# Kernel tuning notes

Measured on AMD Instinct MI355X. Metric: run time of the kernel, lower is better.

The kernel has to match this reference:

```python
import jax, jax.numpy as jnp
from jax import lax
import numpy as np

B, T = 16, 256
E, H, V = 512, 1024, 32000

def setup_inputs() -> dict:
    key = jax.random.key(0)
    ks = jax.random.split(key, 10)
    s = lambda fan_in: 1.0 / np.sqrt(fan_in)
    return {
        "z": jax.random.normal(ks[0], (B, H), dtype=jnp.float32),
        "x": jax.random.randint(ks[1], (B, T), 0, V, dtype=jnp.int64),
        "emb_table": jax.random.normal(ks[2], (V, E), dtype=jnp.float32) * 0.02,
        "W_init": jax.random.uniform(ks[3], (H, H), jnp.float32, -s(H), s(H)),
        "b_init": jnp.zeros((H,), jnp.float32),
        "W_ih": jax.random.uniform(ks[4], (3 * H, E), jnp.float32, -s(H), s(H)),
        "W_hh": jax.random.uniform(ks[5], (3 * H, H), jnp.float32, -s(H), s(H)),
        "b_ih": jax.random.uniform(ks[6], (3 * H,), jnp.float32, -s(H), s(H)),
        "b_hh": jax.random.uniform(ks[7], (3 * H,), jnp.float32, -s(H), s(H)),
        "W_out": jax.random.uniform(ks[8], (V, H), jnp.float32, -s(H), s(H)),
        "b_out": jnp.zeros((V,), jnp.float32),
    }

def reference(z, x, emb_table, W_init, b_init, W_ih, W_hh, b_ih, b_hh, W_out, b_out):
    # h0 = tanh(aff_init_lm(z))
    h0 = jnp.tanh(z @ W_init.T + b_init)  # [B, H]
    xe = emb_table[x]                      # [B, T, E] embedding lookup
    # Precompute input-side gate projections for all timesteps (no recurrence on input side)
    gi_all = jnp.einsum('bte,ge->btg', xe, W_ih) + b_ih  # [B, T, 3H]

    def step(h, gi):
        gh = h @ W_hh.T + b_hh                 # [B, 3H]
        ir, iz, inn = jnp.split(gi, 3, axis=-1)
        hr, hz, hn = jnp.split(gh, 3, axis=-1)
        r = jax.nn.sigmoid(ir + hr)
        zg = jax.nn.sigmoid(iz + hz)
        n = jnp.tanh(inn + r * hn)
        h_new = (1.0 - zg) * n + zg * h
        # Original module emits aff_out_x(h[j]) (state BEFORE consuming token j),
        # so we output the PREVIOUS hidden state at each step.
        return h_new, h

    _, hs_prev = lax.scan(step, h0, jnp.swapaxes(gi_all, 0, 1))  # [T, B, H] = h0..h_{T-1}
    hs = jnp.swapaxes(hs_prev, 0, 1)                              # [B, T, H]
    logits = jnp.einsum('bth,vh->btv', hs, W_out) + b_out         # [B, T, V]
    return logits
```

## Files before the change

kernel.cpp:

```cpp
#include <hip/hip_runtime.h>

typedef __attribute__((ext_vector_type(8))) short bf16x8;
typedef __attribute__((ext_vector_type(8))) unsigned short ushort8;
typedef __attribute__((ext_vector_type(4))) float f32x4;
typedef __attribute__((ext_vector_type(4))) int i32x4;

__device__ __forceinline__ unsigned short f2bf(float f) {
  union { float f; unsigned u; } v; v.f = f;
  unsigned r = (v.u + 0x7FFFu + ((v.u >> 16) & 1u)) >> 16;
  return (unsigned short)r;
}
__device__ __forceinline__ float bf2f(unsigned short h) {
  union { unsigned u; float f; } v; v.u = ((unsigned)h) << 16;
  return v.f;
}
__device__ __forceinline__ float sigm(float x) { return 1.f / (1.f + __expf(-x)); }
__device__ __forceinline__ float tanh_(float x) { return 1.f - 2.f / (__expf(2.f * x) + 1.f); }

__device__ __forceinline__ i32x4 ld_coh_b128(const void* p) {
  i32x4 r;
  asm volatile("global_load_dwordx4 %0, %1, off sc0 sc1" : "=v"(r) : "v"(p) : "memory");
  return r;
}
__device__ __forceinline__ void st_coh_b128(void* p, i32x4 v) {
  asm volatile("global_store_dwordx4 %0, %1, off sc0 sc1" :: "v"(p), "v"(v) : "memory");
}
__device__ __forceinline__ void st_coh_b16(void* p, unsigned v) {
  asm volatile("global_store_short %0, %1, off sc0 sc1" :: "v"(p), "v"(v) : "memory");
}
__device__ __forceinline__ void wait_vm0_fence() {
  asm volatile("s_waitcnt vmcnt(0)" ::: "memory");
  __builtin_amdgcn_sched_barrier(0);
}

#define GLDS(g, l) __builtin_amdgcn_global_load_lds( \
    (const __attribute__((address_space(1))) unsigned int*)(g), \
    (__attribute__((address_space(3))) unsigned int*)(l), 16, 0, 0)

__global__ __launch_bounds__(256) void prep(
    const int* __restrict__ x, const float* __restrict__ emb, unsigned short* __restrict__ xe,
    const float* __restrict__ z, const float* __restrict__ Wi, const float* __restrict__ bi,
    float* __restrict__ h0f, unsigned short* __restrict__ hb16,
    const float* __restrict__ Wih, unsigned short* __restrict__ WihB,
    const float* __restrict__ Wout, unsigned short* __restrict__ WoutB) {
  const int tid = threadIdx.x;
  const unsigned bid = blockIdx.x;
  if (bid < 2048) {
    const int m = (bid << 1) + (tid >> 7);
    const int tok = x[m];
    const int c = tid & 127;
    const float4 v = ((const float4*)(emb + (size_t)tok * 512))[c];
    ushort4 o; o.x = f2bf(v.x); o.y = f2bf(v.y); o.z = f2bf(v.z); o.w = f2bf(v.w);
    ((ushort4*)(xe + (size_t)m * 512))[c] = o;
  } else if (bid < 2112) {
    const int idx = (bid - 2048) * 256 + tid;
    const int b = idx & 15, i = idx >> 4;
    const float4* wr = (const float4*)(Wi + (size_t)i * 1024);
    const float4* zr = (const float4*)(z + (size_t)b * 1024);
    float acc = bi[i];
#pragma unroll 4
    for (int k = 0; k < 256; ++k) {
      float4 w = wr[k], zv = zr[k];
      acc += w.x * zv.x + w.y * zv.y + w.z * zv.z + w.w * zv.w;
    }
    const float h = tanh_(acc);
    h0f[(size_t)b * 1024 + i] = h;
    hb16[((i >> 4) << 8) + (b << 4) + (i & 15)] = f2bf(h);
  } else if (bid < 3648) {
    const int i = (int)(bid - 2112) * 256 + tid;
    const float4 v = ((const float4*)Wih)[i];
    ushort4 o; o.x = f2bf(v.x); o.y = f2bf(v.y); o.z = f2bf(v.z); o.w = f2bf(v.w);
    ((ushort4*)WihB)[i] = o;
  } else {
    for (int i = (int)(bid - 3648) * 256 + tid; i < 32000 * 1024 / 4; i += 512 * 256) {
      const float4 v = ((const float4*)Wout)[i];
      ushort4 o; o.x = f2bf(v.x); o.y = f2bf(v.y); o.z = f2bf(v.z); o.w = f2bf(v.w);
      ((ushort4*)WoutB)[i] = o;
    }
  }
}

__global__ __launch_bounds__(256) void gemm_bt(
    const unsigned short* __restrict__ A, const unsigned short* __restrict__ Bm,
    const float* __restrict__ bias, unsigned short* __restrict__ C,
    int M, int N, int K) {
  __shared__ __align__(16) unsigned short As[128 * 32];
  __shared__ __align__(16) unsigned short Bs[128 * 32];
  const int tid = threadIdx.x;
  const int lane = tid & 63, wave = tid >> 6;
  const int nTM = M >> 7;
  const int nwg = (int)gridDim.x;
  int wg = blockIdx.x;
  if ((nwg & 7) == 0) wg = (wg & 7) * (nwg >> 3) + (wg >> 3);
  const int bm = wg % nTM, bn = wg / nTM;
  const long row0 = (long)bm << 7, col0 = (long)bn << 7;
  const int wm = (wave & 1) << 6, wn = (wave >> 1) << 6;

  f32x4 acc[4][4] = {};

  const int sr = (wave << 4) + (lane >> 2);
  const int sk = (lane & 3) << 3;
  const unsigned short* Abase = A + ((size_t)(row0 + sr)) * K + sk;
  const unsigned short* Bbase = Bm + ((size_t)(col0 + sr)) * K + sk;
  char* ldsA = (char*)As + wave * 1024;
  char* ldsB = (char*)Bs + wave * 1024;

  for (int k0 = 0; k0 < K; k0 += 32) {
    __syncthreads();
    GLDS(Abase + k0, ldsA);
    GLDS(Abase + (size_t)64 * K + k0, ldsA + 4096);
    GLDS(Bbase + k0, ldsB);
    GLDS(Bbase + (size_t)64 * K + k0, ldsB + 4096);
    __syncthreads();
    const int lr = lane & 15, lk = (lane >> 4) << 3;
    bf16x8 af[4], bfr[4];
#pragma unroll
    for (int i = 0; i < 4; ++i) {
      af[i]  = *(const bf16x8*)(As + (wm + i * 16 + lr) * 32 + lk);
      bfr[i] = *(const bf16x8*)(Bs + (wn + i * 16 + lr) * 32 + lk);
    }
#pragma unroll
    for (int i = 0; i < 4; ++i)
#pragma unroll
      for (int j = 0; j < 4; ++j)
        acc[i][j] = __builtin_amdgcn_mfma_f32_16x16x32_bf16(af[i], bfr[j], acc[i][j], 0, 0, 0);
  }

  const int lr = lane & 15, lq = (lane >> 4) << 2;
#pragma unroll
  for (int i = 0; i < 4; ++i) {
#pragma unroll
    for (int q = 0; q < 4; ++q) {
      const long r = row0 + wm + i * 16 + lq + q;
      unsigned short* crow = C + (size_t)r * N;
#pragma unroll
      for (int j = 0; j < 4; ++j) {
        const long cc = col0 + wn + j * 16 + lr;
        crow[cc] = f2bf(acc[i][j][q] + bias[cc]);
      }
    }
  }
}

__global__ __launch_bounds__(512, 1) void mega(
    const float* __restrict__ Whh, const float* __restrict__ bhh,
    const unsigned short* __restrict__ gi, const float* __restrict__ h0f,
    unsigned short* __restrict__ hb16, unsigned short* __restrict__ hs,
    unsigned int* __restrict__ flags, unsigned int* __restrict__ qhead,
    const unsigned short* __restrict__ WoutB, const float* __restrict__ bout,
    float* __restrict__ out) {
  __shared__ __align__(16) char lds[65536];
  const int tid = threadIdx.x, lane = tid & 63, wave = tid >> 6;

  if (blockIdx.x < 64) {
    const int j = blockIdx.x;
    if (tid >= 256) {
      for (int t = 0; t < 256; ++t) { __syncthreads(); if (t < 255) __syncthreads(); }
      __syncthreads();
      return;
    }
    float (*ghp)[16][48] = (float (*)[16][48])lds;
    unsigned short (*hsl)[16] = (unsigned short (*)[16])(lds + 12288);

    const int lr = lane & 15;
    const int hi8 = (lane >> 4) << 3;
    const int kw = wave << 8;

    bf16x8 wf[3][8];
#pragma unroll
    for (int n = 0; n < 3; ++n) {
      const float* wrow = Whh + (size_t)(n * 1024 + (j << 4) + lr) * 1024 + kw + hi8;
#pragma unroll
      for (int ki = 0; ki < 8; ++ki) {
        const float4 u = *(const float4*)(wrow + ki * 32);
        const float4 v = *(const float4*)(wrow + ki * 32 + 4);
        bf16x8 w;
        w[0] = (short)f2bf(u.x); w[1] = (short)f2bf(u.y);
        w[2] = (short)f2bf(u.z); w[3] = (short)f2bf(u.w);
        w[4] = (short)f2bf(v.x); w[5] = (short)f2bf(v.y);
        w[6] = (short)f2bf(v.z); w[7] = (short)f2bf(v.w);
        wf[n][ki] = w;
      }
    }

    const int b = tid >> 4, c = tid & 15;
    const int cg = (j << 4) + c;
    float hreg = h0f[(size_t)b * 1024 + cg];
    const float br = bhh[cg], bz = bhh[1024 + cg], bn = bhh[2048 + cg];

    const unsigned short* gr0 = gi + ((size_t)b * 256 + 0) * 3072;
    float ir = bf2f(gr0[cg]), iz = bf2f(gr0[1024 + cg]), inn = bf2f(gr0[2048 + cg]);

    for (int t = 0; t < 256; ++t) {
      if (t > 0) {
        long guard = 0;
        for (;;) {
          const unsigned f = __hip_atomic_load(&flags[lane << 5], __ATOMIC_RELAXED,
                                               __HIP_MEMORY_SCOPE_AGENT);
          if (__all(f >= (unsigned)t)) break;
          __builtin_amdgcn_s_sleep(1);
          if (++guard > (1L << 20)) break;
        }
      }

      const unsigned short* base = hb16 + ((t & 1) << 14);
      i32x4 hv[8];
#pragma unroll
      for (int ki = 0; ki < 8; ++ki) {
        const int kk = kw + (ki << 5) + hi8;
        hv[ki] = ld_coh_b128(base + ((kk >> 4) << 8) + (lr << 4) + (kk & 15));
      }
      wait_vm0_fence();

      f32x4 acc[3] = {};
#pragma unroll
      for (int ki = 0; ki < 8; ++ki) {
        const bf16x8 af = __builtin_bit_cast(bf16x8, hv[ki]);
#pragma unroll
        for (int n = 0; n < 3; ++n)
          acc[n] = __builtin_amdgcn_mfma_f32_16x16x32_bf16(af, wf[n][ki], acc[n], 0, 0, 0);
      }
#pragma unroll
      for (int n = 0; n < 3; ++n)
#pragma unroll
        for (int q = 0; q < 4; ++q)
          ghp[wave][(lane >> 4) * 4 + q][n * 16 + lr] = acc[n][q];
      __syncthreads();

      const float hr = ghp[0][b][c]      + ghp[1][b][c]      + ghp[2][b][c]      + ghp[3][b][c];
      const float hz = ghp[0][b][16 + c] + ghp[1][b][16 + c] + ghp[2][b][16 + c] + ghp[3][b][16 + c];
      const float hn = ghp[0][b][32 + c] + ghp[1][b][32 + c] + ghp[2][b][32 + c] + ghp[3][b][32 + c];
      const float rg = sigm(ir + hr + br);
      const float zg = sigm(iz + hz + bz);
      const float ng = tanh_(inn + rg * (hn + bn));
      const float hprev = hreg;
      hreg = (1.f - zg) * ng + zg * hprev;

      if (t < 255) {
        hsl[b][c] = f2bf(hreg);
        __syncthreads();
        unsigned short* nb = hb16 + (((t + 1) & 1) << 14) + (j << 8);
        if (tid < 32) {
          const i32x4 v = *(const i32x4*)&hsl[tid >> 1][(tid & 1) << 3];
          st_coh_b128(nb + (tid << 3), v);
        }
        if (wave == 0)
          asm volatile("s_waitcnt vmcnt(0)" ::: "memory");
        if (tid == 0)
          __hip_atomic_store(&flags[j << 5], (unsigned)(t + 1),
                             __ATOMIC_RELAXED, __HIP_MEMORY_SCOPE_AGENT);
      }

      st_coh_b16(hs + ((size_t)((t << 4) + b) << 10) + cg, (unsigned)f2bf(hprev));
      if (t < 255) {
        const unsigned short* gr = gi + ((size_t)b * 256 + (t + 1)) * 3072;
        ir = bf2f(gr[cg]); iz = bf2f(gr[1024 + cg]); inn = bf2f(gr[2048 + cg]);
      }
    }
    asm volatile("s_waitcnt vmcnt(0)" ::: "memory");
    __syncthreads();
    if (tid == 0)
      __hip_atomic_store(&flags[j << 5], 1024u, __ATOMIC_RELAXED, __HIP_MEMORY_SCOPE_AGENT);
    return;
  }

  __shared__ unsigned qk_sh;
  const int wm = wave >> 2, wn = wave & 3;
  const int lr = lane & 15, ko = (lane >> 4) << 4;
  const int arow = tid >> 1, ahalf = (tid & 1) << 5;
  const int awz0 = ((arow << 6) + ahalf) ^ ((arow & 12) << 2);
  const int awz1 = ((arow << 6) + ahalf + 16) ^ ((arow & 12) << 2);
  const int srow = tid >> 2, skb = (tid & 3) << 4;
  const int lq = (lane >> 4) << 2;

  for (;;) {
    if (tid == 0)
      qk_sh = __hip_atomic_fetch_add(qhead, 1u, __ATOMIC_RELAXED, __HIP_MEMORY_SCOPE_AGENT);
    __syncthreads();
    const unsigned k = qk_sh;
    if (k >= 2000u) return;
    const int bm = (int)(k / 125), bn = (int)(k % 125);
    const long row0 = (long)bm << 8, col0 = (long)bn << 8;

    {
      unsigned thr = (unsigned)(16 * bm + 17); if (thr > 255u) thr = 1024u;
      if (wave == 0) {
        long guard = 0;
        for (;;) {
          const unsigned f = __hip_atomic_load(&flags[lane << 5], __ATOMIC_RELAXED,
                                               __HIP_MEMORY_SCOPE_AGENT);
          if (__all(f >= thr)) break;
          __builtin_amdgcn_s_sleep(32);
          if (++guard > (1L << 22)) break;
        }
      }
      __syncthreads();
    }

    const char* Ab = (const char*)hs + ((row0 + arow) << 11) + ahalf;
    auto stageB = [&](int sp, int rr) {
      const int row = (rr << 7) + srow;
      const int kbu = skb ^ ((row & 12) << 2);
      const char* g = (const char*)WoutB + ((col0 + row) << 11) + (sp << 6) + kbu;
      char* l = lds + ((sp & 1) << 15) + 16384 + (rr << 13) + (wave << 10);
      GLDS(g, l);
    };
    auto rdA = [&](int buf, int mrep) {
      const int rt = (wm << 7) + (mrep << 4) + lr;
      const int a = (rt << 6) + ko;
      return *(const bf16x8*)(lds + (buf << 15) + (a ^ ((rt & 12) << 2)));
    };
    auto rdB = [&](int buf, int nrep) {
      const int rt = (wn << 6) + (nrep << 4) + lr;
      const int a = (rt << 6) + ko;
      return *(const bf16x8*)(lds + (buf << 15) + 16384 + (a ^ ((rt & 12) << 2)));
    };

    f32x4 acc[8][4] = {};
    i32x4 rA0 = ld_coh_b128(Ab);
    i32x4 rA1 = ld_coh_b128(Ab + 16);
    stageB(0, 0); stageB(0, 1);

    for (int s = 0; s < 32; ++s) {
      const int buf = s & 1;
      if (s < 31) {
        stageB(s + 1, 0); stageB(s + 1, 1);
        asm volatile("s_waitcnt vmcnt(2)" ::: "memory");
      } else {
        asm volatile("s_waitcnt vmcnt(0)" ::: "memory");
      }
      __builtin_amdgcn_sched_barrier(0);
      *(i32x4*)(lds + (buf << 15) + awz0) = rA0;
      *(i32x4*)(lds + (buf << 15) + awz1) = rA1;
      if (s < 31) {
        rA0 = ld_coh_b128(Ab + ((s + 1) << 6));
        rA1 = ld_coh_b128(Ab + ((s + 1) << 6) + 16);
      }
      asm volatile("s_waitcnt lgkmcnt(0)" ::: "memory");
      __builtin_amdgcn_sched_barrier(0);
      __builtin_amdgcn_s_barrier();

      bf16x8 bfr[4], af[4], af2[4];
#pragma unroll
      for (int n = 0; n < 4; ++n) bfr[n] = rdB(buf, n);
#pragma unroll
      for (int m = 0; m < 4; ++m) af[m] = rdA(buf, m);
      asm volatile("s_waitcnt lgkmcnt(0)" ::: "memory");
      __builtin_amdgcn_sched_barrier(0);
      __builtin_amdgcn_s_setprio(1);
#pragma unroll
      for (int m = 0; m < 4; ++m)
#pragma unroll
        for (int n = 0; n < 4; ++n)
          acc[m][n] = __builtin_amdgcn_mfma_f32_16x16x32_bf16(af[m], bfr[n], acc[m][n], 0, 0, 0);
      __builtin_amdgcn_s_setprio(0);
#pragma unroll
      for (int m = 0; m < 4; ++m) af2[m] = rdA(buf, m + 4);
      asm volatile("s_waitcnt lgkmcnt(0)" ::: "memory");
      __builtin_amdgcn_sched_barrier(0);
      __builtin_amdgcn_s_barrier();
      __builtin_amdgcn_s_setprio(1);
#pragma unroll
      for (int m = 0; m < 4; ++m)
#pragma unroll
        for (int n = 0; n < 4; ++n)
          acc[m + 4][n] = __builtin_amdgcn_mfma_f32_16x16x32_bf16(af2[m], bfr[n], acc[m + 4][n], 0, 0, 0);
      __builtin_amdgcn_s_setprio(0);
    }

#pragma unroll
    for (int mr = 0; mr < 8; ++mr) {
#pragma unroll
      for (int q = 0; q < 4; ++q) {
        const int ar = (int)row0 + (wm << 7) + (mr << 4) + lq + q;
        const int tt = ar >> 4, bb = ar & 15;
        float* crow = out + ((size_t)bb * 256 + tt) * 32000;
#pragma unroll
        for (int nr = 0; nr < 4; ++nr) {
          const long cc = col0 + (wn << 6) + (nr << 4) + lr;
          crow[cc] = acc[mr][nr][q] + bout[cc];
        }
      }
    }
    __syncthreads();
  }
}

extern "C" void kernel_launch(void* const* d_in, const int* in_sizes, int n_in,
                              void* d_out, int out_size, void* d_ws, size_t ws_size,
                              hipStream_t stream) {
  const float* z     = (const float*)d_in[0];
  const int*   x     = (const int*)d_in[1];
  const float* emb   = (const float*)d_in[2];
  const float* Winit = (const float*)d_in[3];
  const float* binit = (const float*)d_in[4];
  const float* Wih   = (const float*)d_in[5];
  const float* Whh   = (const float*)d_in[6];
  const float* bih   = (const float*)d_in[7];
  const float* bhh   = (const float*)d_in[8];
  const float* Wout  = (const float*)d_in[9];
  const float* bout  = (const float*)d_in[10];
  float* out = (float*)d_out;

  char* ws = (char*)d_ws;
  size_t off = 0;
  auto alloc = [&](size_t bytes) { void* p = ws + off; off += (bytes + 255) & ~(size_t)255; return p; };
  unsigned int*   flags = (unsigned int*)alloc(64 * 128);
  unsigned int*   qhead = (unsigned int*)alloc(256);
  unsigned short* xe    = (unsigned short*)alloc((size_t)4096 * 512 * 2);
  unsigned short* WihB  = (unsigned short*)alloc((size_t)3072 * 512 * 2);
  unsigned short* WoutB = (unsigned short*)alloc((size_t)32000 * 1024 * 2);
  unsigned short* giB   = (unsigned short*)alloc((size_t)4096 * 3072 * 2);
  unsigned short* hsB   = (unsigned short*)alloc((size_t)4096 * 1024 * 2);
  float*          h0f   = (float*)alloc((size_t)16 * 1024 * 4);
  unsigned short* hb16  = (unsigned short*)alloc((size_t)2 * 16 * 1024 * 2);
  (void)ws_size; (void)in_sizes; (void)n_in; (void)out_size;

  hipMemsetAsync(flags, 0, 64 * 128 + 256, stream);

  prep<<<dim3(4160), 256, 0, stream>>>(x, emb, xe, z, Winit, binit, h0f, hb16,
                                       Wih, WihB, Wout, WoutB);

  gemm_bt<<<dim3(32 * 24), 256, 0, stream>>>(xe, WihB, bih, giB, 4096, 3072, 512);

  mega<<<dim3(256), 512, 0, stream>>>(Whh, bhh, giB, h0f, hb16, hsB, flags, qhead,
                                      WoutB, bout, out);
}
```

Before: 865.3 us.

## Move W_out bf16 conversion into mega kernel work queue, overlapping recurrence

The fp32-to-bf16 conversion of W_out moves out of the prep kernel and into the persistent mega kernel's dynamic work queue as 512 extra work items. Idle output-GEMM blocks run it while the GRU recurrence blocks execute. A completion counter (wcnt) gates the output-GEMM tiles until all conversion chunks are done. This takes the 128MB read and 64MB write off the serial prep-to-GEMM path, at the cost of competing for memory bandwidth with the recurrence and adding one more atomic poll in the wait loop.

```diff
diff --git a/kernel.cpp b/kernel.cpp
--- a/kernel.cpp
+++ b/kernel.cpp
@@ -4,6 +4,7 @@
 typedef __attribute__((ext_vector_type(8))) unsigned short ushort8;
 typedef __attribute__((ext_vector_type(4))) float f32x4;
 typedef __attribute__((ext_vector_type(4))) int i32x4;
+typedef __attribute__((ext_vector_type(2))) int i32x2;
 
 __device__ __forceinline__ unsigned short f2bf(float f) {
   union { float f; unsigned u; } v; v.f = f;
@@ -25,6 +26,9 @@
 __device__ __forceinline__ void st_coh_b128(void* p, i32x4 v) {
   asm volatile("global_store_dwordx4 %0, %1, off sc0 sc1" :: "v"(p), "v"(v) : "memory");
 }
+__device__ __forceinline__ void st_coh_b64(void* p, i32x2 v) {
+  asm volatile("global_store_dwordx2 %0, %1, off sc0 sc1" :: "v"(p), "v"(v) : "memory");
+}
 __device__ __forceinline__ void st_coh_b16(void* p, unsigned v) {
   asm volatile("global_store_short %0, %1, off sc0 sc1" :: "v"(p), "v"(v) : "memory");
 }
@@ -41,8 +45,7 @@
     const int* __restrict__ x, const float* __restrict__ emb, unsigned short* __restrict__ xe,
     const float* __restrict__ z, const float* __restrict__ Wi, const float* __restrict__ bi,
     float* __restrict__ h0f, unsigned short* __restrict__ hb16,
-    const float* __restrict__ Wih, unsigned short* __restrict__ WihB,
-    const float* __restrict__ Wout, unsigned short* __restrict__ WoutB) {
+    const float* __restrict__ Wih, unsigned short* __restrict__ WihB) {
   const int tid = threadIdx.x;
   const unsigned bid = blockIdx.x;
   if (bid < 2048) {
@@ -66,17 +69,11 @@
     const float h = tanh_(acc);
     h0f[(size_t)b * 1024 + i] = h;
     hb16[((i >> 4) << 8) + (b << 4) + (i & 15)] = f2bf(h);
-  } else if (bid < 3648) {
+  } else {
     const int i = (int)(bid - 2112) * 256 + tid;
     const float4 v = ((const float4*)Wih)[i];
     ushort4 o; o.x = f2bf(v.x); o.y = f2bf(v.y); o.z = f2bf(v.z); o.w = f2bf(v.w);
     ((ushort4*)WihB)[i] = o;
-  } else {
-    for (int i = (int)(bid - 3648) * 256 + tid; i < 32000 * 1024 / 4; i += 512 * 256) {
-      const float4 v = ((const float4*)Wout)[i];
-      ushort4 o; o.x = f2bf(v.x); o.y = f2bf(v.y); o.z = f2bf(v.z); o.w = f2bf(v.w);
-      ((ushort4*)WoutB)[i] = o;
-    }
   }
 }
 
@@ -147,8 +144,9 @@
     const unsigned short* __restrict__ gi, const float* __restrict__ h0f,
     unsigned short* __restrict__ hb16, unsigned short* __restrict__ hs,
     unsigned int* __restrict__ flags, unsigned int* __restrict__ qhead,
-    const unsigned short* __restrict__ WoutB, const float* __restrict__ bout,
-    float* __restrict__ out) {
+    unsigned int* __restrict__ wcnt,
+    const float* __restrict__ Wout, unsigned short* __restrict__ WoutB,
+    const float* __restrict__ bout, float* __restrict__ out) {
   __shared__ __align__(16) char lds[65536];
   const int tid = threadIdx.x, lane = tid & 63, wave = tid >> 6;
 
@@ -278,8 +276,25 @@
       qk_sh = __hip_atomic_fetch_add(qhead, 1u, __ATOMIC_RELAXED, __HIP_MEMORY_SCOPE_AGENT);
     __syncthreads();
     const unsigned k = qk_sh;
-    if (k >= 2000u) return;
-    const int bm = (int)(k / 125), bn = (int)(k % 125);
+    if (k >= 2512u) return;
+
+    if (k < 512u) {
+      const float4* src = (const float4*)Wout;
+      const int base2 = (int)k * 16000;
+      for (int i = base2 + tid; i < base2 + 16000; i += 512) {
+        const float4 v = src[i];
+        ushort4 o; o.x = f2bf(v.x); o.y = f2bf(v.y); o.z = f2bf(v.z); o.w = f2bf(v.w);
+        st_coh_b64((char*)WoutB + (size_t)i * 8, __builtin_bit_cast(i32x2, o));
+      }
+      asm volatile("s_waitcnt vmcnt(0)" ::: "memory");
+      __syncthreads();
+      if (tid == 0)
+        __hip_atomic_fetch_add(wcnt, 1u, __ATOMIC_RELAXED, __HIP_MEMORY_SCOPE_AGENT);
+      continue;
+    }
+
+    const unsigned lk2 = k - 512u;
+    const int bm = (int)(lk2 / 125), bn = (int)(lk2 % 125);
     const long row0 = (long)bm << 8, col0 = (long)bn << 8;
 
     {
@@ -289,7 +304,9 @@
         for (;;) {
           const unsigned f = __hip_atomic_load(&flags[lane << 5], __ATOMIC_RELAXED,
                                                __HIP_MEMORY_SCOPE_AGENT);
-          if (__all(f >= thr)) break;
+          const unsigned w = __hip_atomic_load(wcnt, __ATOMIC_RELAXED,
+                                               __HIP_MEMORY_SCOPE_AGENT);
+          if (__all((f >= thr) && (w >= 512u))) break;
           __builtin_amdgcn_s_sleep(32);
           if (++guard > (1L << 22)) break;
         }
@@ -407,6 +424,7 @@
   auto alloc = [&](size_t bytes) { void* p = ws + off; off += (bytes + 255) & ~(size_t)255; return p; };
   unsigned int*   flags = (unsigned int*)alloc(64 * 128);
   unsigned int*   qhead = (unsigned int*)alloc(256);
+  unsigned int*   wcnt  = (unsigned int*)alloc(256);
   unsigned short* xe    = (unsigned short*)alloc((size_t)4096 * 512 * 2);
   unsigned short* WihB  = (unsigned short*)alloc((size_t)3072 * 512 * 2);
   unsigned short* WoutB = (unsigned short*)alloc((size_t)32000 * 1024 * 2);
@@ -416,13 +434,13 @@
   unsigned short* hb16  = (unsigned short*)alloc((size_t)2 * 16 * 1024 * 2);
   (void)ws_size; (void)in_sizes; (void)n_in; (void)out_size;
 
-  hipMemsetAsync(flags, 0, 64 * 128 + 256, stream);
-
-  prep<<<dim3(4160), 256, 0, stream>>>(x, emb, xe, z, Winit, binit, h0f, hb16,
-                                       Wih, WihB, Wout, WoutB);
+  hipMemsetAsync(flags, 0, 64 * 128 + 256 + 256, stream);
+
+  prep<<<dim3(3648), 256, 0, stream>>>(x, emb, xe, z, Winit, binit, h0f, hb16,
+                                       Wih, WihB);
 
   gemm_bt<<<dim3(32 * 24), 256, 0, stream>>>(xe, WihB, bih, giB, 4096, 3072, 512);
 
   mega<<<dim3(256), 512, 0, stream>>>(Whh, bhh, giB, h0f, hb16, hsB, flags, qhead,
-                                      WoutB, bout, out);
-}
+                                      wcnt, Wout, WoutB, bout, out);
+}
```

Result: slower. 889.4 us (+2.8%).
